# Optimization experiments

Measured on AMD Instinct MI355X. Metric: run time of the kernel, lower is better.

## Reference

```python
import jax, jax.numpy as jnp
import numpy as np

N_HEADS = 1

def setup_inputs() -> dict:
    key = jax.random.key(0)
    kq, kk, kv = jax.random.split(key, 3)
    B, G, H, S = 16, 32, 32, 4096  # batch, n_var (groups), hidden_dim, seq_len
    q = jax.random.normal(kq, (B, G, H, S), dtype=jnp.float32)
    k = jax.random.normal(kk, (B, G, H, S), dtype=jnp.float32)
    v = jax.random.normal(kv, (B, G, H, S), dtype=jnp.float32)
    return {"q": q, "k": k, "v": v}

def reference(q, k, v):
    # q, k, v: (B, G, hidden_dim, S); n_heads = 1 as used by TAMCaD_T
    B, Gq, hidden, S = q.shape
    Gkv = k.shape[1]
    nh = N_HEADS
    dk = hidden // nh
    scale = dk ** -0.5
    qr = q.reshape(B, Gq, nh, dk, S)
    kr = k.reshape(B, Gkv, nh, dk, S)
    vr = v.reshape(B, Gkv, nh, dk, S)
    # logits: (B, nh, S, Gq, Gkv) -- attention over variable pairs per timestep
    logits = scale * jnp.einsum('bghds,bfhds->bhsgf', qr, kr)
    attn = jax.nn.softmax(logits, axis=-1)
    # x: (B, nh, S, Gq, dk)
    x = jnp.einsum('bhsgf,bfhds->bhsgd', attn, vr)
    # permute (0,3,1,4,2) -> (B, Gq, nh, dk, S) -> (B, Gq*nh*dk, S)
    x = x.transpose(0, 3, 1, 4, 2).reshape(B, Gq * nh * dk, S)
    # attentions/logits: mean over heads, then (B, Gq, Gkv, S)
    attentions = attn.mean(axis=1).transpose(0, 2, 3, 1)
    attention_logits = logits.mean(axis=1).transpose(0, 2, 3, 1)
    return x, attentions, attention_logits
```

## Files before the change

kernel.cpp:

```cpp
#include <hip/hip_runtime.h>
#include <hip/hip_bf16.h>


constexpr int S_LEN = 4096;
constexpr int GG = 32;
constexpr int HH = 32;
constexpr int TS = 8;
constexpr float SCALE = 0.17677669529663687f;

__device__ __forceinline__ unsigned bf16pack(float a, float b) {
    unsigned ua = __float_as_uint(a);
    unsigned ub = __float_as_uint(b);
    ua = (ua + 0x7fffu + ((ua >> 16) & 1u)) >> 16;
    ub = (ub + 0x7fffu + ((ub >> 16) & 1u)) >> 16;
    return ua | (ub << 16);
}

__global__ __launch_bounds__(256, 4) void tamcad_fused(
    const float* __restrict__ q, const float* __restrict__ k,
    const float* __restrict__ v, float* __restrict__ x_out,
    float* __restrict__ attn_out, float* __restrict__ logit_out)
{
    __shared__ unsigned k_lds[GG * HH * TS / 2];
    __shared__ unsigned v_lds[GG * HH * TS / 2];

    const int nwg = gridDim.x;
    const int cpx = nwg >> 3;
    const int raw = blockIdx.x;
    const int logical = (raw & 7) * cpx + (raw >> 3);
    const int b  = logical >> 9;
    const int st = logical & 511;
    const int s0 = st * TS;

    const int tid = threadIdx.x;
    const int gt = tid >> 5;
    const int ft = (tid >> 2) & 7;
    const int sp = tid & 3;

    const int baseB = b * (GG * HH);
    const float* qb = q + (size_t)baseB * S_LEN + s0;
    const float* kb = k + (size_t)baseB * S_LEN + s0;
    const float* vb = v + (size_t)baseB * S_LEN + s0;

    for (int r = tid; r < GG * HH; r += 256) {
        const int f = r >> 5, d = r & 31;
        const float4* ks = reinterpret_cast<const float4*>(kb + (size_t)r * S_LEN);
        const float4* vs = reinterpret_cast<const float4*>(vb + (size_t)r * S_LEN);
        float4 k0 = ks[0], k1 = ks[1];
        float4 v0 = vs[0], v1 = vs[1];
        uint4 pk, pv;
        pk.x = bf16pack(k0.x, k0.y); pk.y = bf16pack(k0.z, k0.w);
        pk.z = bf16pack(k1.x, k1.y); pk.w = bf16pack(k1.z, k1.w);
        pv.x = bf16pack(v0.x, v0.y); pv.y = bf16pack(v0.z, v0.w);
        pv.z = bf16pack(v1.x, v1.y); pv.w = bf16pack(v1.z, v1.w);
        const int dk_ = (d + (f >> 2)) & 31;
        *reinterpret_cast<uint4*>(&k_lds[(f * 32 + dk_) * 4]) = pk;
        const int dv_ = ((d & 3) << 3) | (d >> 2);
        *reinterpret_cast<uint4*>(&v_lds[(f * 32 + dv_) * 4]) = pv;
    }
    __syncthreads();

    float acc[4][4][2];
    #pragma unroll
    for (int j = 0; j < 4; ++j)
        #pragma unroll
        for (int i = 0; i < 4; ++i) { acc[j][i][0] = 0.f; acc[j][i][1] = 0.f; }

    const float* qrow[4];
    #pragma unroll
    for (int j = 0; j < 4; ++j)
        qrow[j] = qb + (size_t)((gt * 4 + j) * HH) * S_LEN + sp * 2;

    #pragma unroll 4
    for (int d = 0; d < HH; ++d) {
        float2 qv[4];
        #pragma unroll
        for (int j = 0; j < 4; ++j)
            qv[j] = *reinterpret_cast<const float2*>(qrow[j] + (size_t)d * S_LEN);
        #pragma unroll
        for (int i = 0; i < 4; ++i) {
            const int f = ft * 4 + i;
            const unsigned w = k_lds[(f * 32 + ((d + ft) & 31)) * 4 + sp];
            const float klo = __uint_as_float(w << 16);
            const float khi = __uint_as_float(w & 0xffff0000u);
            #pragma unroll
            for (int j = 0; j < 4; ++j) {
                acc[j][i][0] = fmaf(qv[j].x, klo, acc[j][i][0]);
                acc[j][i][1] = fmaf(qv[j].y, khi, acc[j][i][1]);
            }
        }
    }
    #pragma unroll
    for (int j = 0; j < 4; ++j)
        #pragma unroll
        for (int i = 0; i < 4; ++i) { acc[j][i][0] *= SCALE; acc[j][i][1] *= SCALE; }

    __syncthreads();

    float mx[4][2];
    #pragma unroll
    for (int j = 0; j < 4; ++j) {
        #pragma unroll
        for (int e = 0; e < 2; ++e) {
            float m = fmaxf(fmaxf(acc[j][0][e], acc[j][1][e]),
                            fmaxf(acc[j][2][e], acc[j][3][e]));
            m = fmaxf(m, __shfl_xor(m, 4));
            m = fmaxf(m, __shfl_xor(m, 8));
            m = fmaxf(m, __shfl_xor(m, 16));
            mx[j][e] = m;
        }
    }
    #pragma unroll
    for (int j = 0; j < 4; ++j) {
        const int g = gt * 4 + j;
        #pragma unroll
        for (int i = 0; i < 4; ++i) {
            const int f = ft * 4 + i;
            const size_t o = (size_t)(baseB + g * GG + f) * S_LEN + s0 + sp * 2;
            *reinterpret_cast<float2*>(logit_out + o) = make_float2(acc[j][i][0], acc[j][i][1]);
            acc[j][i][0] = __expf(acc[j][i][0] - mx[j][0]);
            acc[j][i][1] = __expf(acc[j][i][1] - mx[j][1]);
        }
    }
    float inv[4][2];
    #pragma unroll
    for (int j = 0; j < 4; ++j) {
        #pragma unroll
        for (int e = 0; e < 2; ++e) {
            float s = acc[j][0][e] + acc[j][1][e] + acc[j][2][e] + acc[j][3][e];
            s += __shfl_xor(s, 4);
            s += __shfl_xor(s, 8);
            s += __shfl_xor(s, 16);
            inv[j][e] = __builtin_amdgcn_rcpf(s);
        }
    }
    #pragma unroll
    for (int j = 0; j < 4; ++j) {
        const int g = gt * 4 + j;
        #pragma unroll
        for (int i = 0; i < 4; ++i) {
            const int f = ft * 4 + i;
            const float a0 = acc[j][i][0] * inv[j][0];
            const float a1 = acc[j][i][1] * inv[j][1];
            const size_t o = (size_t)(baseB + g * GG + f) * S_LEN + s0 + sp * 2;
            *reinterpret_cast<float2*>(attn_out + o) = make_float2(a0, a1);
            k_lds[(g * 32 + f) * 4 + sp] = bf16pack(a0, a1);
        }
    }
    __syncthreads();

    float xacc[4][4][2];
    #pragma unroll
    for (int j = 0; j < 4; ++j)
        #pragma unroll
        for (int i = 0; i < 4; ++i) { xacc[j][i][0] = 0.f; xacc[j][i][1] = 0.f; }

    const int dt = ft;
    #pragma unroll 4
    for (int f = 0; f < GG; ++f) {
        float alo[4], ahi[4];
        #pragma unroll
        for (int j = 0; j < 4; ++j) {
            const unsigned w = k_lds[((gt * 4 + j) * 32 + f) * 4 + sp];
            alo[j] = __uint_as_float(w << 16);
            ahi[j] = __uint_as_float(w & 0xffff0000u);
        }
        #pragma unroll
        for (int i = 0; i < 4; ++i) {
            const unsigned w = v_lds[(f * 32 + i * 8 + dt) * 4 + sp];
            const float vlo = __uint_as_float(w << 16);
            const float vhi = __uint_as_float(w & 0xffff0000u);
            #pragma unroll
            for (int j = 0; j < 4; ++j) {
                xacc[j][i][0] = fmaf(alo[j], vlo, xacc[j][i][0]);
                xacc[j][i][1] = fmaf(ahi[j], vhi, xacc[j][i][1]);
            }
        }
    }
    #pragma unroll
    for (int j = 0; j < 4; ++j) {
        const int g = gt * 4 + j;
        #pragma unroll
        for (int i = 0; i < 4; ++i) {
            const int d = dt * 4 + i;
            const size_t o = (size_t)(baseB + g * HH + d) * S_LEN + s0 + sp * 2;
            *reinterpret_cast<float2*>(x_out + o) = make_float2(xacc[j][i][0], xacc[j][i][1]);
        }
    }
}

extern "C" void kernel_launch(void* const* d_in, const int* in_sizes, int n_in,
                              void* d_out, int out_size, void* d_ws, size_t ws_size,
                              hipStream_t stream) {
    const float* q = (const float*)d_in[0];
    const float* k = (const float*)d_in[1];
    const float* v = (const float*)d_in[2];
    float* out = (float*)d_out;
    const int n = in_sizes[0];
    const int B = n / (GG * HH * S_LEN);
    float* x_out     = out;
    float* attn_out  = out + (size_t)n;
    float* logit_out = out + (size_t)2 * n;
    const int nwg = B * (S_LEN / TS);
    tamcad_fused<<<dim3(nwg), dim3(256), 0, stream>>>(q, k, v, x_out, attn_out, logit_out);
}
```

Baseline: 589.0 us.

## Double sequence tile to 16 with 512 threads and swizzled vectorized LDS attention layout

Raises the per-block sequence tile from 8 to 16 timesteps and the block size to 512 threads, so each row load moves 64 bytes and half as many workgroups are launched. The K/V shared-memory layout gains an XOR swizzle to limit bank conflicts at the wider stride. Attention weights are held in registers and then written as uint4 into a transposed, swizzled LDS layout so the second matmul reads them with one vector load per f. LDS use per block doubles and the launch bound of 512x4 raises register pressure, which may reduce occupancy.

```diff
diff --git a/kernel.cpp b/kernel.cpp
--- a/kernel.cpp
+++ b/kernel.cpp
@@ -5,7 +5,7 @@
 constexpr int S_LEN = 4096;
 constexpr int GG = 32;
 constexpr int HH = 32;
-constexpr int TS = 8;
+constexpr int TS = 16;
 constexpr float SCALE = 0.17677669529663687f;
 
 __device__ __forceinline__ unsigned bf16pack(float a, float b) {
@@ -16,47 +16,55 @@
     return ua | (ub << 16);
 }
 
-__global__ __launch_bounds__(256, 4) void tamcad_fused(
+__global__ __launch_bounds__(512, 4) void tamcad_fused(
     const float* __restrict__ q, const float* __restrict__ k,
     const float* __restrict__ v, float* __restrict__ x_out,
     float* __restrict__ attn_out, float* __restrict__ logit_out)
 {
-    __shared__ unsigned k_lds[GG * HH * TS / 2];
-    __shared__ unsigned v_lds[GG * HH * TS / 2];
+    __shared__ __align__(16) unsigned k_lds[GG * HH * TS / 2];
+    __shared__ __align__(16) unsigned v_lds[GG * HH * TS / 2];
 
     const int nwg = gridDim.x;
     const int cpx = nwg >> 3;
     const int raw = blockIdx.x;
     const int logical = (raw & 7) * cpx + (raw >> 3);
-    const int b  = logical >> 9;
-    const int st = logical & 511;
+    const int b  = logical >> 8;
+    const int st = logical & 255;
     const int s0 = st * TS;
 
     const int tid = threadIdx.x;
-    const int gt = tid >> 5;
-    const int ft = (tid >> 2) & 7;
-    const int sp = tid & 3;
+    const int gt = tid >> 6;
+    const int ft = (tid >> 3) & 7;
+    const int sp = tid & 7;
 
     const int baseB = b * (GG * HH);
     const float* qb = q + (size_t)baseB * S_LEN + s0;
     const float* kb = k + (size_t)baseB * S_LEN + s0;
     const float* vb = v + (size_t)baseB * S_LEN + s0;
 
-    for (int r = tid; r < GG * HH; r += 256) {
+    for (int r = tid; r < GG * HH; r += 512) {
         const int f = r >> 5, d = r & 31;
         const float4* ks = reinterpret_cast<const float4*>(kb + (size_t)r * S_LEN);
         const float4* vs = reinterpret_cast<const float4*>(vb + (size_t)r * S_LEN);
-        float4 k0 = ks[0], k1 = ks[1];
-        float4 v0 = vs[0], v1 = vs[1];
-        uint4 pk, pv;
-        pk.x = bf16pack(k0.x, k0.y); pk.y = bf16pack(k0.z, k0.w);
-        pk.z = bf16pack(k1.x, k1.y); pk.w = bf16pack(k1.z, k1.w);
-        pv.x = bf16pack(v0.x, v0.y); pv.y = bf16pack(v0.z, v0.w);
-        pv.z = bf16pack(v1.x, v1.y); pv.w = bf16pack(v1.z, v1.w);
-        const int dk_ = (d + (f >> 2)) & 31;
-        *reinterpret_cast<uint4*>(&k_lds[(f * 32 + dk_) * 4]) = pk;
-        const int dv_ = ((d & 3) << 3) | (d >> 2);
-        *reinterpret_cast<uint4*>(&v_lds[(f * 32 + dv_) * 4]) = pv;
+        float4 k0 = ks[0], k1 = ks[1], k2 = ks[2], k3 = ks[3];
+        float4 v0 = vs[0], v1 = vs[1], v2 = vs[2], v3 = vs[3];
+        uint4 kl, kh, vl, vh;
+        kl.x = bf16pack(k0.x, k0.y); kl.y = bf16pack(k0.z, k0.w);
+        kl.z = bf16pack(k1.x, k1.y); kl.w = bf16pack(k1.z, k1.w);
+        kh.x = bf16pack(k2.x, k2.y); kh.y = bf16pack(k2.z, k2.w);
+        kh.z = bf16pack(k3.x, k3.y); kh.w = bf16pack(k3.z, k3.w);
+        vl.x = bf16pack(v0.x, v0.y); vl.y = bf16pack(v0.z, v0.w);
+        vl.z = bf16pack(v1.x, v1.y); vl.w = bf16pack(v1.z, v1.w);
+        vh.x = bf16pack(v2.x, v2.y); vh.y = bf16pack(v2.z, v2.w);
+        vh.z = bf16pack(v3.x, v3.y); vh.w = bf16pack(v3.z, v3.w);
+        const int rk = f * 32 + ((d + (f >> 2)) & 31);
+        const int xk = rk & 4;
+        *reinterpret_cast<uint4*>(&k_lds[rk * 8 + xk])       = kl;
+        *reinterpret_cast<uint4*>(&k_lds[rk * 8 + (4 ^ xk)]) = kh;
+        const int rv = f * 32 + (((d & 3) << 3) | (d >> 2));
+        const int xv = rv & 4;
+        *reinterpret_cast<uint4*>(&v_lds[rv * 8 + xv])       = vl;
+        *reinterpret_cast<uint4*>(&v_lds[rv * 8 + (4 ^ xv)]) = vh;
     }
     __syncthreads();
 
@@ -77,10 +85,11 @@
         #pragma unroll
         for (int j = 0; j < 4; ++j)
             qv[j] = *reinterpret_cast<const float2*>(qrow[j] + (size_t)d * S_LEN);
-        #pragma unroll
-        for (int i = 0; i < 4; ++i) {
-            const int f = ft * 4 + i;
-            const unsigned w = k_lds[(f * 32 + ((d + ft) & 31)) * 4 + sp];
+        const int dd = (d + ft) & 31;
+        const int so = sp ^ (dd & 4);
+        #pragma unroll
+        for (int i = 0; i < 4; ++i) {
+            const unsigned w = k_lds[((ft * 4 + i) * 32 + dd) * 8 + so];
             const float klo = __uint_as_float(w << 16);
             const float khi = __uint_as_float(w & 0xffff0000u);
             #pragma unroll
@@ -95,8 +104,6 @@
         #pragma unroll
         for (int i = 0; i < 4; ++i) { acc[j][i][0] *= SCALE; acc[j][i][1] *= SCALE; }
 
-    __syncthreads();
-
     float mx[4][2];
     #pragma unroll
     for (int j = 0; j < 4; ++j) {
@@ -104,9 +111,9 @@
         for (int e = 0; e < 2; ++e) {
             float m = fmaxf(fmaxf(acc[j][0][e], acc[j][1][e]),
                             fmaxf(acc[j][2][e], acc[j][3][e]));
-            m = fmaxf(m, __shfl_xor(m, 4));
             m = fmaxf(m, __shfl_xor(m, 8));
             m = fmaxf(m, __shfl_xor(m, 16));
+            m = fmaxf(m, __shfl_xor(m, 32));
             mx[j][e] = m;
         }
     }
@@ -128,12 +135,13 @@
         #pragma unroll
         for (int e = 0; e < 2; ++e) {
             float s = acc[j][0][e] + acc[j][1][e] + acc[j][2][e] + acc[j][3][e];
-            s += __shfl_xor(s, 4);
             s += __shfl_xor(s, 8);
             s += __shfl_xor(s, 16);
+            s += __shfl_xor(s, 32);
             inv[j][e] = __builtin_amdgcn_rcpf(s);
         }
     }
+    unsigned apack[4][4];
     #pragma unroll
     for (int j = 0; j < 4; ++j) {
         const int g = gt * 4 + j;
@@ -144,10 +152,18 @@
             const float a1 = acc[j][i][1] * inv[j][1];
             const size_t o = (size_t)(baseB + g * GG + f) * S_LEN + s0 + sp * 2;
             *reinterpret_cast<float2*>(attn_out + o) = make_float2(a0, a1);
-            k_lds[(g * 32 + f) * 4 + sp] = bf16pack(a0, a1);
+            apack[i][j] = bf16pack(a0, a1);
         }
     }
     __syncthreads();
+    #pragma unroll
+    for (int i = 0; i < 4; ++i) {
+        const int f = ft * 4 + i;
+        uint4 w;
+        w.x = apack[i][0]; w.y = apack[i][1]; w.z = apack[i][2]; w.w = apack[i][3];
+        *reinterpret_cast<uint4*>(&k_lds[((f * 8 + gt) * 8 + (sp ^ ft)) * 4]) = w;
+    }
+    __syncthreads();
 
     float xacc[4][4][2];
     #pragma unroll
@@ -156,18 +172,20 @@
         for (int i = 0; i < 4; ++i) { xacc[j][i][0] = 0.f; xacc[j][i][1] = 0.f; }
 
     const int dt = ft;
+    const int sov = sp ^ (dt & 4);
     #pragma unroll 4
     for (int f = 0; f < GG; ++f) {
+        const int fp = f >> 2;
+        const uint4 wa = *reinterpret_cast<const uint4*>(
+            &k_lds[((f * 8 + gt) * 8 + (sp ^ fp)) * 4]);
         float alo[4], ahi[4];
-        #pragma unroll
-        for (int j = 0; j < 4; ++j) {
-            const unsigned w = k_lds[((gt * 4 + j) * 32 + f) * 4 + sp];
-            alo[j] = __uint_as_float(w << 16);
-            ahi[j] = __uint_as_float(w & 0xffff0000u);
-        }
-        #pragma unroll
-        for (int i = 0; i < 4; ++i) {
-            const unsigned w = v_lds[(f * 32 + i * 8 + dt) * 4 + sp];
+        alo[0] = __uint_as_float(wa.x << 16); ahi[0] = __uint_as_float(wa.x & 0xffff0000u);
+        alo[1] = __uint_as_float(wa.y << 16); ahi[1] = __uint_as_float(wa.y & 0xffff0000u);
+        alo[2] = __uint_as_float(wa.z << 16); ahi[2] = __uint_as_float(wa.z & 0xffff0000u);
+        alo[3] = __uint_as_float(wa.w << 16); ahi[3] = __uint_as_float(wa.w & 0xffff0000u);
+        #pragma unroll
+        for (int i = 0; i < 4; ++i) {
+            const unsigned w = v_lds[(f * 32 + i * 8 + dt) * 8 + sov];
             const float vlo = __uint_as_float(w << 16);
             const float vhi = __uint_as_float(w & 0xffff0000u);
             #pragma unroll
@@ -202,5 +220,5 @@
     float* attn_out  = out + (size_t)n;
     float* logit_out = out + (size_t)2 * n;
     const int nwg = B * (S_LEN / TS);
-    tamcad_fused<<<dim3(nwg), dim3(256), 0, stream>>>(q, k, v, x_out, attn_out, logit_out);
+    tamcad_fused<<<dim3(nwg), dim3(512), 0, stream>>>(q, k, v, x_out, attn_out, logit_out);
 }
```

After: 513.3 us. 1.15x faster.

## Restructure fused attention to one thread per (query group, timestep) with 16-step tiles

Applied to the files above, without the earlier changes.

Doubles the timestep tile to 16 and the block to 512 threads, with each thread owning one (g, s) pair. Each thread keeps its q column and its full logits row in registers, so softmax needs no cross-lane shuffles. K and V are staged as bf16 pairs along d in LDS with an XOR swizzle and read back as uint4 vectors. The cost is much higher register pressure from the 32-wide q, logits and x arrays, plus narrower per-thread scalar global stores.

```diff
diff --git a/kernel.cpp b/kernel.cpp
--- a/kernel.cpp
+++ b/kernel.cpp
@@ -1,11 +1,10 @@
 #include <hip/hip_runtime.h>
-#include <hip/hip_bf16.h>
 
 
 constexpr int S_LEN = 4096;
 constexpr int GG = 32;
 constexpr int HH = 32;
-constexpr int TS = 8;
+constexpr int TS = 16;
 constexpr float SCALE = 0.17677669529663687f;
 
 __device__ __forceinline__ unsigned bf16pack(float a, float b) {
@@ -16,177 +15,141 @@
     return ua | (ub << 16);
 }
 
-__global__ __launch_bounds__(256, 4) void tamcad_fused(
+__global__ __launch_bounds__(512, 4) void tamcad_fused(
     const float* __restrict__ q, const float* __restrict__ k,
     const float* __restrict__ v, float* __restrict__ x_out,
     float* __restrict__ attn_out, float* __restrict__ logit_out)
 {
-    __shared__ unsigned k_lds[GG * HH * TS / 2];
-    __shared__ unsigned v_lds[GG * HH * TS / 2];
+    __shared__ __align__(16) unsigned lds[GG * TS * 16 * 2];
 
     const int nwg = gridDim.x;
     const int cpx = nwg >> 3;
     const int raw = blockIdx.x;
     const int logical = (raw & 7) * cpx + (raw >> 3);
-    const int b  = logical >> 9;
-    const int st = logical & 511;
+    const int b  = logical >> 8;
+    const int st = logical & 255;
     const int s0 = st * TS;
 
     const int tid = threadIdx.x;
-    const int gt = tid >> 5;
-    const int ft = (tid >> 2) & 7;
-    const int sp = tid & 3;
+    const int g = tid >> 4;
+    const int s = tid & 15;
 
     const int baseB = b * (GG * HH);
     const float* qb = q + (size_t)baseB * S_LEN + s0;
     const float* kb = k + (size_t)baseB * S_LEN + s0;
     const float* vb = v + (size_t)baseB * S_LEN + s0;
 
-    for (int r = tid; r < GG * HH; r += 256) {
-        const int f = r >> 5, d = r & 31;
-        const float4* ks = reinterpret_cast<const float4*>(kb + (size_t)r * S_LEN);
-        const float4* vs = reinterpret_cast<const float4*>(vb + (size_t)r * S_LEN);
-        float4 k0 = ks[0], k1 = ks[1];
-        float4 v0 = vs[0], v1 = vs[1];
-        uint4 pk, pv;
-        pk.x = bf16pack(k0.x, k0.y); pk.y = bf16pack(k0.z, k0.w);
-        pk.z = bf16pack(k1.x, k1.y); pk.w = bf16pack(k1.z, k1.w);
-        pv.x = bf16pack(v0.x, v0.y); pv.y = bf16pack(v0.z, v0.w);
-        pv.z = bf16pack(v1.x, v1.y); pv.w = bf16pack(v1.z, v1.w);
-        const int dk_ = (d + (f >> 2)) & 31;
-        *reinterpret_cast<uint4*>(&k_lds[(f * 32 + dk_) * 4]) = pk;
-        const int dv_ = ((d & 3) << 3) | (d >> 2);
-        *reinterpret_cast<uint4*>(&v_lds[(f * 32 + dv_) * 4]) = pv;
-    }
-    __syncthreads();
+    float qreg[32];
+    #pragma unroll
+    for (int d = 0; d < 32; ++d)
+        qreg[d] = qb[(size_t)(g * HH + d) * S_LEN + s];
 
-    float acc[4][4][2];
-    #pragma unroll
-    for (int j = 0; j < 4; ++j)
+    {
+        const int fst = g;
+        const int dp  = s;
+        const int dpl = dp & 3;
+        const int dph = (dp >> 2) << 2;
+        unsigned* const wbase = &lds[fst * 256 + dpl];
+        unsigned* const was[4] = { wbase + (dph ^ 0),  wbase + (dph ^ 4),
+                                   wbase + (dph ^ 8),  wbase + (dph ^ 12) };
+
+        const float4* k0p = reinterpret_cast<const float4*>(kb + (size_t)(fst * HH + 2 * dp)     * S_LEN);
+        const float4* k1p = reinterpret_cast<const float4*>(kb + (size_t)(fst * HH + 2 * dp + 1) * S_LEN);
+        const float4* v0p = reinterpret_cast<const float4*>(vb + (size_t)(fst * HH + 2 * dp)     * S_LEN);
+        const float4* v1p = reinterpret_cast<const float4*>(vb + (size_t)(fst * HH + 2 * dp + 1) * S_LEN);
+
+        float r0[16], r1[16], t0[16], t1[16];
         #pragma unroll
-        for (int i = 0; i < 4; ++i) { acc[j][i][0] = 0.f; acc[j][i][1] = 0.f; }
-
-    const float* qrow[4];
-    #pragma unroll
-    for (int j = 0; j < 4; ++j)
-        qrow[j] = qb + (size_t)((gt * 4 + j) * HH) * S_LEN + sp * 2;
-
-    #pragma unroll 4
-    for (int d = 0; d < HH; ++d) {
-        float2 qv[4];
+        for (int sq = 0; sq < 4; ++sq) {
+            *reinterpret_cast<float4*>(&r0[sq * 4]) = k0p[sq];
+            *reinterpret_cast<float4*>(&r1[sq * 4]) = k1p[sq];
+            *reinterpret_cast<float4*>(&t0[sq * 4]) = v0p[sq];
+            *reinterpret_cast<float4*>(&t1[sq * 4]) = v1p[sq];
+        }
         #pragma unroll
-        for (int j = 0; j < 4; ++j)
-            qv[j] = *reinterpret_cast<const float2*>(qrow[j] + (size_t)d * S_LEN);
-        #pragma unroll
-        for (int i = 0; i < 4; ++i) {
-            const int f = ft * 4 + i;
-            const unsigned w = k_lds[(f * 32 + ((d + ft) & 31)) * 4 + sp];
-            const float klo = __uint_as_float(w << 16);
-            const float khi = __uint_as_float(w & 0xffff0000u);
-            #pragma unroll
-            for (int j = 0; j < 4; ++j) {
-                acc[j][i][0] = fmaf(qv[j].x, klo, acc[j][i][0]);
-                acc[j][i][1] = fmaf(qv[j].y, khi, acc[j][i][1]);
-            }
-        }
-    }
-    #pragma unroll
-    for (int j = 0; j < 4; ++j)
-        #pragma unroll
-        for (int i = 0; i < 4; ++i) { acc[j][i][0] *= SCALE; acc[j][i][1] *= SCALE; }
-
-    __syncthreads();
-
-    float mx[4][2];
-    #pragma unroll
-    for (int j = 0; j < 4; ++j) {
-        #pragma unroll
-        for (int e = 0; e < 2; ++e) {
-            float m = fmaxf(fmaxf(acc[j][0][e], acc[j][1][e]),
-                            fmaxf(acc[j][2][e], acc[j][3][e]));
-            m = fmaxf(m, __shfl_xor(m, 4));
-            m = fmaxf(m, __shfl_xor(m, 8));
-            m = fmaxf(m, __shfl_xor(m, 16));
-            mx[j][e] = m;
-        }
-    }
-    #pragma unroll
-    for (int j = 0; j < 4; ++j) {
-        const int g = gt * 4 + j;
-        #pragma unroll
-        for (int i = 0; i < 4; ++i) {
-            const int f = ft * 4 + i;
-            const size_t o = (size_t)(baseB + g * GG + f) * S_LEN + s0 + sp * 2;
-            *reinterpret_cast<float2*>(logit_out + o) = make_float2(acc[j][i][0], acc[j][i][1]);
-            acc[j][i][0] = __expf(acc[j][i][0] - mx[j][0]);
-            acc[j][i][1] = __expf(acc[j][i][1] - mx[j][1]);
-        }
-    }
-    float inv[4][2];
-    #pragma unroll
-    for (int j = 0; j < 4; ++j) {
-        #pragma unroll
-        for (int e = 0; e < 2; ++e) {
-            float s = acc[j][0][e] + acc[j][1][e] + acc[j][2][e] + acc[j][3][e];
-            s += __shfl_xor(s, 4);
-            s += __shfl_xor(s, 8);
-            s += __shfl_xor(s, 16);
-            inv[j][e] = __builtin_amdgcn_rcpf(s);
-        }
-    }
-    #pragma unroll
-    for (int j = 0; j < 4; ++j) {
-        const int g = gt * 4 + j;
-        #pragma unroll
-        for (int i = 0; i < 4; ++i) {
-            const int f = ft * 4 + i;
-            const float a0 = acc[j][i][0] * inv[j][0];
-            const float a1 = acc[j][i][1] * inv[j][1];
-            const size_t o = (size_t)(baseB + g * GG + f) * S_LEN + s0 + sp * 2;
-            *reinterpret_cast<float2*>(attn_out + o) = make_float2(a0, a1);
-            k_lds[(g * 32 + f) * 4 + sp] = bf16pack(a0, a1);
+        for (int ss = 0; ss < 16; ++ss) {
+            unsigned* wp = was[(ss >> 1) & 3] + ss * 16;
+            wp[0]    = bf16pack(r0[ss], r1[ss]);
+            wp[8192] = bf16pack(t0[ss], t1[ss]);
         }
     }
     __syncthreads();
 
-    float xacc[4][4][2];
+    const int xs = (s >> 1) & 3;
+    const unsigned* const rp0 = &lds[s * 16 + ((0 ^ xs) << 2)];
+    const unsigned* const rp1 = &lds[s * 16 + ((1 ^ xs) << 2)];
+    const unsigned* const rp2 = &lds[s * 16 + ((2 ^ xs) << 2)];
+    const unsigned* const rp3 = &lds[s * 16 + ((3 ^ xs) << 2)];
+
+    float l[32];
+#define QKW(u, d0) { \
+        const float klo_ = __uint_as_float((u) << 16); \
+        const float khi_ = __uint_as_float((u) & 0xffff0000u); \
+        a0 = fmaf(qreg[d0], klo_, a0); \
+        a1 = fmaf(qreg[(d0) + 1], khi_, a1); }
     #pragma unroll
-    for (int j = 0; j < 4; ++j)
-        #pragma unroll
-        for (int i = 0; i < 4; ++i) { xacc[j][i][0] = 0.f; xacc[j][i][1] = 0.f; }
+    for (int f = 0; f < 32; ++f) {
+        float a0 = 0.f, a1 = 0.f;
+        const uint4 c0 = *reinterpret_cast<const uint4*>(rp0 + f * 256);
+        const uint4 c1 = *reinterpret_cast<const uint4*>(rp1 + f * 256);
+        const uint4 c2 = *reinterpret_cast<const uint4*>(rp2 + f * 256);
+        const uint4 c3 = *reinterpret_cast<const uint4*>(rp3 + f * 256);
+        QKW(c0.x,  0) QKW(c0.y,  2) QKW(c0.z,  4) QKW(c0.w,  6)
+        QKW(c1.x,  8) QKW(c1.y, 10) QKW(c1.z, 12) QKW(c1.w, 14)
+        QKW(c2.x, 16) QKW(c2.y, 18) QKW(c2.z, 20) QKW(c2.w, 22)
+        QKW(c3.x, 24) QKW(c3.y, 26) QKW(c3.z, 28) QKW(c3.w, 30)
+        l[f] = (a0 + a1) * SCALE;
+        logit_out[(size_t)(baseB + g * GG + f) * S_LEN + s0 + s] = l[f];
+    }
+#undef QKW
 
-    const int dt = ft;
-    #pragma unroll 4
-    for (int f = 0; f < GG; ++f) {
-        float alo[4], ahi[4];
-        #pragma unroll
-        for (int j = 0; j < 4; ++j) {
-            const unsigned w = k_lds[((gt * 4 + j) * 32 + f) * 4 + sp];
-            alo[j] = __uint_as_float(w << 16);
-            ahi[j] = __uint_as_float(w & 0xffff0000u);
-        }
-        #pragma unroll
-        for (int i = 0; i < 4; ++i) {
-            const unsigned w = v_lds[(f * 32 + i * 8 + dt) * 4 + sp];
-            const float vlo = __uint_as_float(w << 16);
-            const float vhi = __uint_as_float(w & 0xffff0000u);
-            #pragma unroll
-            for (int j = 0; j < 4; ++j) {
-                xacc[j][i][0] = fmaf(alo[j], vlo, xacc[j][i][0]);
-                xacc[j][i][1] = fmaf(ahi[j], vhi, xacc[j][i][1]);
-            }
-        }
+    float tm[16];
+    #pragma unroll
+    for (int i = 0; i < 16; ++i) tm[i] = fmaxf(l[2 * i], l[2 * i + 1]);
+    #pragma unroll
+    for (int i = 0; i < 8; ++i) tm[i] = fmaxf(tm[i], tm[i + 8]);
+    #pragma unroll
+    for (int i = 0; i < 4; ++i) tm[i] = fmaxf(tm[i], tm[i + 4]);
+    const float m = fmaxf(fmaxf(tm[0], tm[1]), fmaxf(tm[2], tm[3]));
+
+    float ts4[4] = {0.f, 0.f, 0.f, 0.f};
+    #pragma unroll
+    for (int f = 0; f < 32; ++f) {
+        l[f] = __expf(l[f] - m);
+        ts4[f & 3] += l[f];
     }
+    const float sum = (ts4[0] + ts4[1]) + (ts4[2] + ts4[3]);
+    const float inv = __builtin_amdgcn_rcpf(sum);
     #pragma unroll
-    for (int j = 0; j < 4; ++j) {
-        const int g = gt * 4 + j;
-        #pragma unroll
-        for (int i = 0; i < 4; ++i) {
-            const int d = dt * 4 + i;
-            const size_t o = (size_t)(baseB + g * HH + d) * S_LEN + s0 + sp * 2;
-            *reinterpret_cast<float2*>(x_out + o) = make_float2(xacc[j][i][0], xacc[j][i][1]);
-        }
+    for (int f = 0; f < 32; ++f) {
+        l[f] *= inv;
+        attn_out[(size_t)(baseB + g * GG + f) * S_LEN + s0 + s] = l[f];
     }
+
+    float xa[32];
+    #pragma unroll
+    for (int d = 0; d < 32; ++d) xa[d] = 0.f;
+#define PVW(u, d0) { \
+        const float vlo_ = __uint_as_float((u) << 16); \
+        const float vhi_ = __uint_as_float((u) & 0xffff0000u); \
+        xa[d0] = fmaf(av, vlo_, xa[d0]); \
+        xa[(d0) + 1] = fmaf(av, vhi_, xa[(d0) + 1]); }
+    #pragma unroll
+    for (int f = 0; f < 32; ++f) {
+        const float av = l[f];
+        const uint4 c0 = *reinterpret_cast<const uint4*>(rp0 + 8192 + f * 256);
+        const uint4 c1 = *reinterpret_cast<const uint4*>(rp1 + 8192 + f * 256);
+        const uint4 c2 = *reinterpret_cast<const uint4*>(rp2 + 8192 + f * 256);
+        const uint4 c3 = *reinterpret_cast<const uint4*>(rp3 + 8192 + f * 256);
+        PVW(c0.x,  0) PVW(c0.y,  2) PVW(c0.z,  4) PVW(c0.w,  6)
+        PVW(c1.x,  8) PVW(c1.y, 10) PVW(c1.z, 12) PVW(c1.w, 14)
+        PVW(c2.x, 16) PVW(c2.y, 18) PVW(c2.z, 20) PVW(c2.w, 22)
+        PVW(c3.x, 24) PVW(c3.y, 26) PVW(c3.z, 28) PVW(c3.w, 30)
+    }
+#undef PVW
+    #pragma unroll
+    for (int d = 0; d < 32; ++d)
+        x_out[(size_t)(baseB + g * HH + d) * S_LEN + s0 + s] = xa[d];
 }
 
 extern "C" void kernel_launch(void* const* d_in, const int* in_sizes, int n_in,
@@ -202,5 +165,5 @@
     float* attn_out  = out + (size_t)n;
     float* logit_out = out + (size_t)2 * n;
     const int nwg = B * (S_LEN / TS);
-    tamcad_fused<<<dim3(nwg), dim3(256), 0, stream>>>(q, k, v, x_out, attn_out, logit_out);
+    tamcad_fused<<<dim3(nwg), dim3(512), 0, stream>>>(q, k, v, x_out, attn_out, logit_out);
 }
```

New measurement: 535.9 us. -9.0%, faster.
